# Kernel optimization log

Measured on AMD Instinct MI355X. Metric: run time of the kernel, lower is better.

Reference implementation:

```python
import jax, jax.numpy as jnp
import numpy as np
import math

B, N, DIM = 4, 2048, 768
HEADS, DIM_HEAD = 12, 64
SCALE = math.sqrt(DIM_HEAD)


def setup_inputs() -> dict:
    key = jax.random.key(0)
    ks = jax.random.split(key, 5)
    inner = HEADS * DIM_HEAD
    x = jax.random.normal(ks[0], (B, N, DIM), dtype=jnp.float32)
    # Linear weights stored as [in, out] so y = x @ W (equivalent to torch Linear with W.T)
    w_q = jax.random.normal(ks[1], (DIM, inner), dtype=jnp.float32) * 0.02
    w_k = jax.random.normal(ks[2], (DIM, inner), dtype=jnp.float32) * 0.02
    w_v = jax.random.normal(ks[3], (DIM, inner), dtype=jnp.float32) * 0.02
    w_o = jax.random.normal(ks[4], (inner, DIM), dtype=jnp.float32) * 0.02
    b_o = jnp.zeros((DIM,), dtype=jnp.float32)
    return {"x": x, "w_q": w_q, "w_k": w_k, "w_v": w_v, "w_o": w_o, "b_o": b_o}


def _split_heads(t):
    # [b, n, h*d] -> [b, h, n, d]
    b, n, _ = t.shape
    return t.reshape(b, n, HEADS, DIM_HEAD).transpose(0, 2, 1, 3)


def reference(x, w_q, w_k, w_v, w_o, b_o):
    # context = x (self-attention, kv_include_self=False)
    q = _split_heads(x @ w_q)  # [b,h,n,d]
    k = _split_heads(x @ w_k)
    v = _split_heads(x @ w_v)
    scores = jnp.einsum("bhnd,bhmd->bhnm", q, k) / SCALE  # [b,h,n,n]
    attn = jax.nn.softmax(scores, axis=-1)  # dropout p=0 -> identity
    h = jnp.einsum("bhnm,bhmd->bhnd", attn, v)  # [b,h,n,d]
    H = h.transpose(0, 2, 1, 3).reshape(x.shape[0], x.shape[1], HEADS * DIM_HEAD)
    out = H @ w_o + b_o
    return out
```

## Files before the change

kernel.cpp:

```cpp
#include <hip/hip_runtime.h>
#include <hip/hip_bf16.h>
#include <cstdint>
#include <cstddef>

#define HEADS 12
#define DHEAD 64
#define SEQ   2048
#define DIMM  768
#define BATCH 4
#define MROWS (BATCH*SEQ)
#define BH    (BATCH*HEADS)
#define SCL_Q 0.18033688011112042f

typedef __attribute__((ext_vector_type(8))) short short8;
typedef __attribute__((ext_vector_type(4))) short short4v;
typedef __attribute__((ext_vector_type(4))) float floatx4;

__device__ __forceinline__ unsigned short f2bf(float f) {
    union { float f; uint32_t u; } v; v.f = f;
    uint32_t u = v.u;
    u += 0x7fffu + ((u >> 16) & 1u);
    return (unsigned short)(u >> 16);
}
__device__ __forceinline__ float bf2f(unsigned short h) {
    union { uint32_t u; float f; } v; v.u = ((uint32_t)h) << 16;
    return v.f;
}
__device__ __forceinline__ uint32_t pkbf(float a, float b) {
    __hip_bfloat162 h = __float22bfloat162_rn(make_float2(a, b));
    uint32_t u; __builtin_memcpy(&u, &h, 4); return u;
}
__device__ __forceinline__ float fexp2(float x) {
#if __has_builtin(__builtin_amdgcn_exp2f)
    return __builtin_amdgcn_exp2f(x);
#else
    return exp2f(x);
#endif
}

#if __has_builtin(__builtin_amdgcn_global_load_lds)
#define HAVE_GLDS 1
__device__ __forceinline__ void glds16(const unsigned short* g, unsigned short* l) {
    __builtin_amdgcn_global_load_lds(
        (const __attribute__((address_space(1))) unsigned int*)g,
        (__attribute__((address_space(3))) unsigned int*)l, 16, 0, 0);
}
#else
#define HAVE_GLDS 0
#endif

__device__ __forceinline__ int detect_f32(const uint32_t* xw, int tid) {
    __shared__ int cnt_;
    if (tid == 0) cnt_ = 0;
    __syncthreads();
    uint32_t w = xw[(size_t)(tid & 255) * 4096];
    float av = fabsf(bf2f((unsigned short)(w & 0xFFFFu)));
    atomicAdd(&cnt_, (av >= 9.0949e-13f && av <= 256.0f) ? 1 : 0);
    __syncthreads();
    return (cnt_ < 192) ? 1 : 0;
}

__global__ __launch_bounds__(256) void prep(
    const void* __restrict__ x,
    const void* __restrict__ wq, const void* __restrict__ wk,
    const void* __restrict__ wv, const void* __restrict__ wo,
    unsigned short* __restrict__ xc,
    unsigned short* __restrict__ wtq, unsigned short* __restrict__ wtk,
    unsigned short* __restrict__ wtv, unsigned short* __restrict__ wto)
{
    const int tid = threadIdx.x;
    const int isf32 = detect_f32((const uint32_t*)x, tid);
    const int blk = blockIdx.x;

    if (blk < 2304) {
        __shared__ unsigned short tile[32][33];
        const int m = blk / 576, rr = blk % 576;
        const void* src; unsigned short* dst;
        switch (m) {
            case 0: src = wq; dst = wtq; break;
            case 1: src = wk; dst = wtk; break;
            case 2: src = wv; dst = wtv; break;
            default: src = wo; dst = wto; break;
        }
        const float* srcf = (const float*)src;
        const unsigned short* srcs = (const unsigned short*)src;
        const int tx = tid & 31, ty = tid >> 5;
        const int k0 = (rr % 24) * 32;
        const int n0 = (rr / 24) * 32;
        #pragma unroll
        for (int it = 0; it < 4; it++) {
            int r = ty + it * 8;
            size_t idx = (size_t)(k0 + r) * DIMM + n0 + tx;
            tile[r][tx] = isf32 ? f2bf(srcf[idx]) : srcs[idx];
        }
        __syncthreads();
        #pragma unroll
        for (int it = 0; it < 4; it++) {
            int r = ty + it * 8;
            dst[(size_t)(n0 + r) * DIMM + k0 + tx] = tile[tx][r];
        }
    } else {
        const size_t i0 = ((size_t)(blk - 2304) * 256 + tid) * 8;
        if (isf32) {
            const float* xf = (const float*)x;
            float4 a = *(const float4*)&xf[i0];
            float4 b = *(const float4*)&xf[i0 + 4];
            short8 s = { (short)f2bf(a.x), (short)f2bf(a.y), (short)f2bf(a.z), (short)f2bf(a.w),
                         (short)f2bf(b.x), (short)f2bf(b.y), (short)f2bf(b.z), (short)f2bf(b.w) };
            *(short8*)&xc[i0] = s;
        } else {
            *(short8*)&xc[i0] = *(const short8*)&((const unsigned short*)x)[i0];
        }
    }
}

__global__ __launch_bounds__(256) void gemm_bt(
    const unsigned short* __restrict__ A,
    const unsigned short* __restrict__ Wt0,
    const unsigned short* __restrict__ Wt1,
    const unsigned short* __restrict__ Wt2,
    void* __restrict__ O0, void* __restrict__ O1, void* __restrict__ O2,
    const void* __restrict__ bias,
    const uint32_t* __restrict__ xsample,
    int mode_base)
{
    const int mode = mode_base + blockIdx.z;
    const unsigned short* Wt = (mode == 1) ? Wt1 : (mode == 2) ? Wt2 : Wt0;
    void* OutV               = (mode == 1) ? O1  : (mode == 2) ? O2  : O0;
    unsigned short* Out16 = (unsigned short*)OutV;
    float* Outf           = (float*)OutV;

    int isf32 = 0;
    if (mode == 3) isf32 = detect_f32(xsample, threadIdx.x);

    __shared__ unsigned short As[128 * 64];
    __shared__ unsigned short Bs[128 * 64];

    const int tid  = threadIdx.x;
    const int wid  = tid >> 6;
    const int lane = tid & 63;
    const int l16  = lane & 15;
    const int quad = lane >> 4;
    const int wm   = wid & 1;
    const int wn   = wid >> 1;
    const int bm   = blockIdx.x * 128;
    const int bn   = blockIdx.y * 128;
    const bool swap = (mode != 2);

    floatx4 acc[4][4];
    #pragma unroll
    for (int i = 0; i < 4; i++)
        #pragma unroll
        for (int j = 0; j < 4; j++)
            acc[i][j] = floatx4{0.f, 0.f, 0.f, 0.f};

    for (int kk = 0; kk < DIMM; kk += 64) {
        #pragma unroll
        for (int t = 0; t < 4; t++) {
            const int c  = t * 256 + tid;
            const int r  = c >> 3;
            const int lc = (((c & 7) ^ (r & 7))) * 8;
#if HAVE_GLDS
            glds16(&A [(size_t)(bm + r) * DIMM + kk + lc], &As[(t * 256 + wid * 64) * 8]);
            glds16(&Wt[(size_t)(bn + r) * DIMM + kk + lc], &Bs[(t * 256 + wid * 64) * 8]);
#else
            *(short8*)&As[c * 8] = *(const short8*)&A [(size_t)(bm + r) * DIMM + kk + lc];
            *(short8*)&Bs[c * 8] = *(const short8*)&Wt[(size_t)(bn + r) * DIMM + kk + lc];
#endif
        }
        __syncthreads();
        #pragma unroll
        for (int ks = 0; ks < 2; ks++) {
            const int ph = ((ks * 4 + quad) ^ (l16 & 7)) * 8;
            short8 xa[4], wb[4];
            #pragma unroll
            for (int t = 0; t < 4; t++)
                xa[t] = *(const short8*)&As[(wm * 64 + t * 16 + l16) * 64 + ph];
            #pragma unroll
            for (int t = 0; t < 4; t++)
                wb[t] = *(const short8*)&Bs[(wn * 64 + t * 16 + l16) * 64 + ph];
            if (swap) {
                #pragma unroll
                for (int mt = 0; mt < 4; mt++)
                    #pragma unroll
                    for (int nt = 0; nt < 4; nt++)
                        acc[mt][nt] = __builtin_amdgcn_mfma_f32_16x16x32_bf16(
                            wb[mt], xa[nt], acc[mt][nt], 0, 0, 0);
            } else {
                #pragma unroll
                for (int mt = 0; mt < 4; mt++)
                    #pragma unroll
                    for (int nt = 0; nt < 4; nt++)
                        acc[mt][nt] = __builtin_amdgcn_mfma_f32_16x16x32_bf16(
                            xa[mt], wb[nt], acc[mt][nt], 0, 0, 0);
            }
        }
        __syncthreads();
    }

    if (!swap) {
        #pragma unroll
        for (int nt = 0; nt < 4; nt++) {
            const int gcol = bn + wn * 64 + nt * 16 + l16;
            #pragma unroll
            for (int mt = 0; mt < 4; mt++) {
                const int grow0 = bm + wm * 64 + mt * 16 + quad * 4;
                const int b = grow0 >> 11, n0 = grow0 & 2047;
                const int h = gcol >> 6,  d  = gcol & 63;
                size_t addr = ((size_t)(b * HEADS + h) * DHEAD + d) * SEQ + n0;
                short4v pk = { (short)f2bf(acc[mt][nt][0]), (short)f2bf(acc[mt][nt][1]),
                               (short)f2bf(acc[mt][nt][2]), (short)f2bf(acc[mt][nt][3]) };
                *(short4v*)&Out16[addr] = pk;
            }
        }
    } else {
        #pragma unroll
        for (int nt = 0; nt < 4; nt++) {
            const int grow = bm + wm * 64 + nt * 16 + l16;
            #pragma unroll
            for (int mt = 0; mt < 4; mt++) {
                const int gcol0 = bn + wn * 64 + mt * 16 + quad * 4;
                float v0 = acc[mt][nt][0], v1 = acc[mt][nt][1];
                float v2 = acc[mt][nt][2], v3 = acc[mt][nt][3];
                if (mode == 0) { v0 *= SCL_Q; v1 *= SCL_Q; v2 *= SCL_Q; v3 *= SCL_Q; }
                if (mode == 3) {
                    if (isf32) {
                        float4 bv = *(const float4*)&((const float*)bias)[gcol0];
                        float4 o = { v0 + bv.x, v1 + bv.y, v2 + bv.z, v3 + bv.w };
                        *(float4*)&Outf[(size_t)grow * DIMM + gcol0] = o;
                    } else {
                        const unsigned short* bb = &((const unsigned short*)bias)[gcol0];
                        short4v pk = { (short)f2bf(v0 + bf2f(bb[0])),
                                       (short)f2bf(v1 + bf2f(bb[1])),
                                       (short)f2bf(v2 + bf2f(bb[2])),
                                       (short)f2bf(v3 + bf2f(bb[3])) };
                        *(short4v*)&Out16[(size_t)grow * DIMM + gcol0] = pk;
                    }
                } else {
                    const int b = grow >> 11, n = grow & 2047;
                    const int h = gcol0 >> 6, d = gcol0 & 63;
                    size_t addr = ((size_t)(b * HEADS + h) * SEQ + n) * DHEAD + d;
                    short4v pk = { (short)f2bf(v0), (short)f2bf(v1),
                                   (short)f2bf(v2), (short)f2bf(v3) };
                    *(short4v*)&Out16[addr] = pk;
                }
            }
        }
    }
}

__global__ __launch_bounds__(256, 3) void attn(
    const unsigned short* __restrict__ Q,
    const unsigned short* __restrict__ K,
    const unsigned short* __restrict__ Vt,
    unsigned short* __restrict__ Hout)
{
    __shared__ unsigned short Ks[64 * 72];
    __shared__ unsigned short Vs[64 * 72];
    __shared__ unsigned short Ps[8][16 * 72];

    const int tid  = threadIdx.x;
    const int wid  = tid >> 6;
    const int lane = tid & 63;
    const int l16  = lane & 15;
    const int quad = lane >> 4;

    const int bh = blockIdx.x % BH;
    const int qt = blockIdx.x / BH;

    short8 qf[2][2];
    #pragma unroll
    for (int t = 0; t < 2; t++) {
        const int qrow = qt * 128 + wid * 32 + t * 16 + l16;
        const size_t qbase = ((size_t)bh * SEQ + qrow) * DHEAD;
        qf[t][0] = *(const short8*)&Q[qbase + quad * 8];
        qf[t][1] = *(const short8*)&Q[qbase + 32 + quad * 8];
    }

    const short8 ones = { (short)0x3F80, (short)0x3F80, (short)0x3F80, (short)0x3F80,
                          (short)0x3F80, (short)0x3F80, (short)0x3F80, (short)0x3F80 };

    floatx4 ot[2][4];
    floatx4 acc_l[2];
    #pragma unroll
    for (int t = 0; t < 2; t++) {
        acc_l[t] = floatx4{0.f, 0.f, 0.f, 0.f};
        #pragma unroll
        for (int i = 0; i < 4; i++) ot[t][i] = floatx4{0.f, 0.f, 0.f, 0.f};
    }

    const size_t kbase = (size_t)bh * SEQ * DHEAD;
    const size_t vbase = (size_t)bh * DHEAD * SEQ;

    short8 rk[2], rv[2];
    #pragma unroll
    for (int j = 0; j < 2; j++) {
        const int c = tid + j * 256, r = c >> 3, c8 = (c & 7) * 8;
        rk[j] = *(const short8*)&K[kbase + (size_t)r * DHEAD + c8];
        rv[j] = *(const short8*)&Vt[vbase + (size_t)r * SEQ + c8];
    }

    short8 vfr[2][4];
    short8 pfr[2][2];

    for (int kt = 0; kt < SEQ / 64; kt++) {
        if (kt > 0) {
            #pragma unroll
            for (int ks = 0; ks < 2; ks++) {
                #pragma unroll
                for (int dt = 0; dt < 4; dt++)
                    vfr[ks][dt] = *(const short8*)&Vs[(dt * 16 + l16) * 72 + ks * 32 + quad * 8];
                #pragma unroll
                for (int t = 0; t < 2; t++)
                    pfr[ks][t] = *(const short8*)&Ps[wid * 2 + t][l16 * 72 + ks * 32 + quad * 8];
            }
        }
        __syncthreads();
        #pragma unroll
        for (int j = 0; j < 2; j++) {
            const int c = tid + j * 256, r = c >> 3, c8 = (c & 7) * 8;
            *(short8*)&Ks[r * 72 + c8] = rk[j];
            *(short8*)&Vs[r * 72 + c8] = rv[j];
        }
        __syncthreads();
        if (kt + 1 < SEQ / 64) {
            #pragma unroll
            for (int j = 0; j < 2; j++) {
                const int c = tid + j * 256, r = c >> 3, c8 = (c & 7) * 8;
                rk[j] = *(const short8*)&K[kbase + (size_t)((kt + 1) * 64 + r) * DHEAD + c8];
                rv[j] = *(const short8*)&Vt[vbase + (size_t)r * SEQ + (kt + 1) * 64 + c8];
            }
        }

        uint2 pk[2][4];
        #pragma unroll
        for (int mt = 0; mt < 4; mt++) {
            short8 kf0 = *(const short8*)&Ks[(mt * 16 + l16) * 72 + quad * 8];
            short8 kf1 = *(const short8*)&Ks[(mt * 16 + l16) * 72 + 32 + quad * 8];
            #pragma unroll
            for (int t = 0; t < 2; t++) {
                floatx4 a = floatx4{0.f, 0.f, 0.f, 0.f};
                a = __builtin_amdgcn_mfma_f32_16x16x32_bf16(kf0, qf[t][0], a, 0, 0, 0);
                a = __builtin_amdgcn_mfma_f32_16x16x32_bf16(kf1, qf[t][1], a, 0, 0, 0);
                pk[t][mt] = (uint2){ pkbf(fexp2(a[0]), fexp2(a[1])),
                                     pkbf(fexp2(a[2]), fexp2(a[3])) };
            }
        }

        if (kt > 0) {
            #pragma unroll
            for (int ks = 0; ks < 2; ks++) {
                #pragma unroll
                for (int t = 0; t < 2; t++) {
                    #pragma unroll
                    for (int dt = 0; dt < 4; dt++)
                        ot[t][dt] = __builtin_amdgcn_mfma_f32_16x16x32_bf16(
                            vfr[ks][dt], pfr[ks][t], ot[t][dt], 0, 0, 0);
                    acc_l[t] = __builtin_amdgcn_mfma_f32_16x16x32_bf16(
                        ones, pfr[ks][t], acc_l[t], 0, 0, 0);
                }
            }
        }

        #pragma unroll
        for (int t = 0; t < 2; t++)
            #pragma unroll
            for (int mt = 0; mt < 4; mt++)
                *(uint2*)&Ps[wid * 2 + t][l16 * 72 + mt * 16 + quad * 4] = pk[t][mt];
    }

    {
        #pragma unroll
        for (int ks = 0; ks < 2; ks++) {
            #pragma unroll
            for (int dt = 0; dt < 4; dt++)
                vfr[ks][dt] = *(const short8*)&Vs[(dt * 16 + l16) * 72 + ks * 32 + quad * 8];
            #pragma unroll
            for (int t = 0; t < 2; t++)
                pfr[ks][t] = *(const short8*)&Ps[wid * 2 + t][l16 * 72 + ks * 32 + quad * 8];
        }
        #pragma unroll
        for (int ks = 0; ks < 2; ks++)
            #pragma unroll
            for (int t = 0; t < 2; t++) {
                #pragma unroll
                for (int dt = 0; dt < 4; dt++)
                    ot[t][dt] = __builtin_amdgcn_mfma_f32_16x16x32_bf16(
                        vfr[ks][dt], pfr[ks][t], ot[t][dt], 0, 0, 0);
                acc_l[t] = __builtin_amdgcn_mfma_f32_16x16x32_bf16(
                    ones, pfr[ks][t], acc_l[t], 0, 0, 0);
            }
    }

    const int b = bh / HEADS, h = bh % HEADS;
    #pragma unroll
    for (int t = 0; t < 2; t++) {
        const float inv_l = 1.0f / acc_l[t][0];
        unsigned short* Pw = Ps[wid * 2 + t];
        #pragma unroll
        for (int dt = 0; dt < 4; dt++) {
            uint2 pk2 = { pkbf(ot[t][dt][0] * inv_l, ot[t][dt][1] * inv_l),
                          pkbf(ot[t][dt][2] * inv_l, ot[t][dt][3] * inv_l) };
            *(uint2*)&Pw[l16 * 72 + dt * 16 + quad * 4] = pk2;
        }
        const int q_r   = lane >> 2;
        const int dpart = (lane & 3) * 16;
        short8 h0 = *(const short8*)&Pw[q_r * 72 + dpart];
        short8 h1 = *(const short8*)&Pw[q_r * 72 + dpart + 8];
        const int growg = b * SEQ + qt * 128 + wid * 32 + t * 16 + q_r;
        const size_t oaddr = (size_t)growg * DIMM + h * DHEAD + dpart;
        *(short8*)&Hout[oaddr] = h0;
        *(short8*)&Hout[oaddr + 8] = h1;
    }
}

extern "C" void kernel_launch(void* const* d_in, const int* in_sizes, int n_in,
                              void* d_out, int out_size, void* d_ws, size_t ws_size,
                              hipStream_t stream)
{
    (void)in_sizes; (void)n_in; (void)out_size;
    const void* x  = d_in[0];
    const void* wq = d_in[1];
    const void* wk = d_in[2];
    const void* wv = d_in[3];
    const void* wo = d_in[4];
    const void* bo = d_in[5];

    char* ws = (char*)d_ws;
    const size_t SZ_QKV = (size_t)MROWS * DIMM * sizeof(unsigned short);
    const size_t SZ_W   = (size_t)DIMM * DIMM * sizeof(unsigned short);
    const size_t need = 5 * SZ_QKV + 4 * SZ_W;
    if (ws_size < need) return;

    unsigned short* xc   = (unsigned short*)(ws);
    unsigned short* Qws  = (unsigned short*)(ws + 1 * SZ_QKV);
    unsigned short* Kws  = (unsigned short*)(ws + 2 * SZ_QKV);
    unsigned short* Vtws = (unsigned short*)(ws + 3 * SZ_QKV);
    unsigned short* Hws  = (unsigned short*)(ws + 4 * SZ_QKV);
    unsigned short* Wtq  = (unsigned short*)(ws + 5 * SZ_QKV);
    unsigned short* Wtk  = (unsigned short*)(ws + 5 * SZ_QKV + SZ_W);
    unsigned short* Wtv  = (unsigned short*)(ws + 5 * SZ_QKV + 2 * SZ_W);
    unsigned short* Wto  = (unsigned short*)(ws + 5 * SZ_QKV + 3 * SZ_W);

    hipLaunchKernelGGL(prep, dim3(2304 + MROWS * DIMM / 2048), dim3(256), 0, stream,
                       x, wq, wk, wv, wo, xc, Wtq, Wtk, Wtv, Wto);
    hipLaunchKernelGGL(gemm_bt, dim3(64, 6, 3), dim3(256), 0, stream,
                       xc, Wtq, Wtk, Wtv, (void*)Qws, (void*)Kws, (void*)Vtws,
                       bo, (const uint32_t*)x, 0);
    hipLaunchKernelGGL(attn, dim3(BH * (SEQ / 128)), dim3(256), 0, stream,
                       Qws, Kws, Vtws, Hws);
    hipLaunchKernelGGL(gemm_bt, dim3(64, 6, 1), dim3(256), 0, stream,
                       Hws, Wto, Wto, Wto, d_out, d_out, d_out,
                       bo, (const uint32_t*)x, 3);
}
```

Measured before the change: 242.9 us.

## Load K/V MFMA fragments directly from global memory, dropping LDS staging

The attention kernel no longer stages K and V tiles in shared memory behind block-wide barriers. Each wave now reads its K and V^T MFMA fragments straight from global memory, relying on L2/L1 for reuse across the four waves. The software pipeline that deferred the PV product by one iteration is removed, so PV now runs in the same iteration using only the per-wave P buffer in LDS. This cuts __syncthreads and LDS traffic but multiplies global/cache load requests by four and exposes load latency without explicit prefetch.

```diff
diff --git a/kernel.cpp b/kernel.cpp
--- a/kernel.cpp
+++ b/kernel.cpp
@@ -255,8 +255,6 @@
     const unsigned short* __restrict__ Vt,
     unsigned short* __restrict__ Hout)
 {
-    __shared__ unsigned short Ks[64 * 72];
-    __shared__ unsigned short Vs[64 * 72];
     __shared__ unsigned short Ps[8][16 * 72];
 
     const int tid  = threadIdx.x;
@@ -289,107 +287,56 @@
         for (int i = 0; i < 4; i++) ot[t][i] = floatx4{0.f, 0.f, 0.f, 0.f};
     }
 
-    const size_t kbase = (size_t)bh * SEQ * DHEAD;
-    const size_t vbase = (size_t)bh * DHEAD * SEQ;
-
-    short8 rk[2], rv[2];
-    #pragma unroll
-    for (int j = 0; j < 2; j++) {
-        const int c = tid + j * 256, r = c >> 3, c8 = (c & 7) * 8;
-        rk[j] = *(const short8*)&K[kbase + (size_t)r * DHEAD + c8];
-        rv[j] = *(const short8*)&Vt[vbase + (size_t)r * SEQ + c8];
-    }
-
-    short8 vfr[2][4];
-    short8 pfr[2][2];
+    const unsigned short* Kp = &K[(size_t)bh * SEQ * DHEAD + (size_t)l16 * DHEAD + quad * 8];
+    const unsigned short* Vp = &Vt[(size_t)bh * DHEAD * SEQ + (size_t)l16 * SEQ + quad * 8];
 
     for (int kt = 0; kt < SEQ / 64; kt++) {
-        if (kt > 0) {
-            #pragma unroll
-            for (int ks = 0; ks < 2; ks++) {
-                #pragma unroll
-                for (int dt = 0; dt < 4; dt++)
-                    vfr[ks][dt] = *(const short8*)&Vs[(dt * 16 + l16) * 72 + ks * 32 + quad * 8];
-                #pragma unroll
-                for (int t = 0; t < 2; t++)
-                    pfr[ks][t] = *(const short8*)&Ps[wid * 2 + t][l16 * 72 + ks * 32 + quad * 8];
-            }
-        }
-        __syncthreads();
-        #pragma unroll
-        for (int j = 0; j < 2; j++) {
-            const int c = tid + j * 256, r = c >> 3, c8 = (c & 7) * 8;
-            *(short8*)&Ks[r * 72 + c8] = rk[j];
-            *(short8*)&Vs[r * 72 + c8] = rv[j];
-        }
-        __syncthreads();
-        if (kt + 1 < SEQ / 64) {
-            #pragma unroll
-            for (int j = 0; j < 2; j++) {
-                const int c = tid + j * 256, r = c >> 3, c8 = (c & 7) * 8;
-                rk[j] = *(const short8*)&K[kbase + (size_t)((kt + 1) * 64 + r) * DHEAD + c8];
-                rv[j] = *(const short8*)&Vt[vbase + (size_t)r * SEQ + (kt + 1) * 64 + c8];
-            }
-        }
+        short8 kf[4][2];
+        #pragma unroll
+        for (int mt = 0; mt < 4; mt++) {
+            const unsigned short* kr = Kp + (size_t)(kt * 64 + mt * 16) * DHEAD;
+            kf[mt][0] = *(const short8*)(kr);
+            kf[mt][1] = *(const short8*)(kr + 32);
+        }
+        short8 vf[2][4];
+        #pragma unroll
+        for (int ks = 0; ks < 2; ks++)
+            #pragma unroll
+            for (int dt = 0; dt < 4; dt++)
+                vf[ks][dt] = *(const short8*)(Vp + (size_t)(dt * 16) * SEQ + kt * 64 + ks * 32);
 
         uint2 pk[2][4];
         #pragma unroll
         for (int mt = 0; mt < 4; mt++) {
-            short8 kf0 = *(const short8*)&Ks[(mt * 16 + l16) * 72 + quad * 8];
-            short8 kf1 = *(const short8*)&Ks[(mt * 16 + l16) * 72 + 32 + quad * 8];
             #pragma unroll
             for (int t = 0; t < 2; t++) {
                 floatx4 a = floatx4{0.f, 0.f, 0.f, 0.f};
-                a = __builtin_amdgcn_mfma_f32_16x16x32_bf16(kf0, qf[t][0], a, 0, 0, 0);
-                a = __builtin_amdgcn_mfma_f32_16x16x32_bf16(kf1, qf[t][1], a, 0, 0, 0);
+                a = __builtin_amdgcn_mfma_f32_16x16x32_bf16(kf[mt][0], qf[t][0], a, 0, 0, 0);
+                a = __builtin_amdgcn_mfma_f32_16x16x32_bf16(kf[mt][1], qf[t][1], a, 0, 0, 0);
                 pk[t][mt] = (uint2){ pkbf(fexp2(a[0]), fexp2(a[1])),
                                      pkbf(fexp2(a[2]), fexp2(a[3])) };
             }
         }
 
-        if (kt > 0) {
-            #pragma unroll
-            for (int ks = 0; ks < 2; ks++) {
-                #pragma unroll
-                for (int t = 0; t < 2; t++) {
-                    #pragma unroll
-                    for (int dt = 0; dt < 4; dt++)
-                        ot[t][dt] = __builtin_amdgcn_mfma_f32_16x16x32_bf16(
-                            vfr[ks][dt], pfr[ks][t], ot[t][dt], 0, 0, 0);
-                    acc_l[t] = __builtin_amdgcn_mfma_f32_16x16x32_bf16(
-                        ones, pfr[ks][t], acc_l[t], 0, 0, 0);
-                }
-            }
-        }
-
         #pragma unroll
         for (int t = 0; t < 2; t++)
             #pragma unroll
             for (int mt = 0; mt < 4; mt++)
                 *(uint2*)&Ps[wid * 2 + t][l16 * 72 + mt * 16 + quad * 4] = pk[t][mt];
-    }
-
-    {
+
         #pragma unroll
         for (int ks = 0; ks < 2; ks++) {
             #pragma unroll
-            for (int dt = 0; dt < 4; dt++)
-                vfr[ks][dt] = *(const short8*)&Vs[(dt * 16 + l16) * 72 + ks * 32 + quad * 8];
-            #pragma unroll
-            for (int t = 0; t < 2; t++)
-                pfr[ks][t] = *(const short8*)&Ps[wid * 2 + t][l16 * 72 + ks * 32 + quad * 8];
-        }
-        #pragma unroll
-        for (int ks = 0; ks < 2; ks++)
-            #pragma unroll
             for (int t = 0; t < 2; t++) {
+                short8 pf = *(const short8*)&Ps[wid * 2 + t][l16 * 72 + ks * 32 + quad * 8];
                 #pragma unroll
                 for (int dt = 0; dt < 4; dt++)
                     ot[t][dt] = __builtin_amdgcn_mfma_f32_16x16x32_bf16(
-                        vfr[ks][dt], pfr[ks][t], ot[t][dt], 0, 0, 0);
+                        vf[ks][dt], pf, ot[t][dt], 0, 0, 0);
                 acc_l[t] = __builtin_amdgcn_mfma_f32_16x16x32_bf16(
-                    ones, pfr[ks][t], acc_l[t], 0, 0, 0);
+                    ones, pf, acc_l[t], 0, 0, 0);
             }
+        }
     }
 
     const int b = bh / HEADS, h = bh % HEADS;
```

Result: slower. 339.6 us (+39.8%).
